# Kernel tuning notes

Measured on AMD Instinct MI355X. Metric: run time of the kernel, lower is better.

## Reference

```python
import jax, jax.numpy as jnp
import numpy as np

B, T, C = 2, 2048, 1024
NH = 16

def setup_inputs() -> dict:
    key = jax.random.key(0)
    ks = jax.random.split(key, 5)
    s = 0.02
    return {
        "x": jax.random.normal(ks[0], (B, T, C), dtype=jnp.float32),
        "w_attn": jax.random.normal(ks[1], (C, 3 * C), dtype=jnp.float32) * s,
        "b_attn": jax.random.normal(ks[2], (3 * C,), dtype=jnp.float32) * s,
        "w_proj": jax.random.normal(ks[3], (C, C), dtype=jnp.float32) * s,
        "b_proj": jax.random.normal(ks[4], (C,), dtype=jnp.float32) * s,
        "n_heads": NH,
    }

def reference(x, w_attn, b_attn, w_proj, b_proj, n_heads):
    Bx, Tx, Cx = x.shape
    hd = Cx // n_heads
    qkv = x @ w_attn + b_attn                      # [B,T,3C]
    q, k, v = jnp.split(qkv, 3, axis=-1)
    # [B,T,H,hd] -> [B,H,T,hd]
    q = q.reshape(Bx, Tx, n_heads, hd).transpose(0, 2, 1, 3)
    k = k.reshape(Bx, Tx, n_heads, hd).transpose(0, 2, 1, 3)
    v = v.reshape(Bx, Tx, n_heads, hd).transpose(0, 2, 1, 3)
    scale = 1.0 / np.sqrt(hd).astype(np.float32)
    att = jnp.einsum('bhqd,bhkd->bhqk', q, k) * scale   # [B,H,T,T]
    causal = jnp.tril(jnp.ones((Tx, Tx), dtype=bool))
    att = jnp.where(causal[None, None], att, -jnp.inf)
    att = jax.nn.softmax(att, axis=-1)
    y = jnp.einsum('bhqk,bhkd->bhqd', att, v)            # [B,H,T,hd]
    y = y.transpose(0, 2, 1, 3).reshape(Bx, Tx, Cx)
    return y @ w_proj + b_proj
```

## Files before the change

kernel.cpp:

```cpp
#include <hip/hip_runtime.h>

typedef __bf16 bf16x8 __attribute__((ext_vector_type(8)));
typedef float  f32x4  __attribute__((ext_vector_type(4)));

#define MFMA_BF16(a, b, c) __builtin_amdgcn_mfma_f32_16x16x32_bf16((a), (b), (c), 0, 0, 0)
#define NEG_INF (-1e30f)
#define SCL 0.18033688f

__device__ __forceinline__ void gld16(const void* g, void* l) {
  __builtin_amdgcn_global_load_lds(
      (const __attribute__((address_space(1))) void*)g,
      (__attribute__((address_space(3))) void*)l, 16, 0, 0);
}

__global__ void cast_f32_bf16(const float* __restrict__ in,
                              __bf16* __restrict__ out, int n) {
  int i = (blockIdx.x * 256 + threadIdx.x) * 8;
  if (i >= n) return;
  float4 a = *(const float4*)&in[i];
  float4 b = *(const float4*)&in[i + 4];
  bf16x8 v;
  v[0] = (__bf16)a.x; v[1] = (__bf16)a.y; v[2] = (__bf16)a.z; v[3] = (__bf16)a.w;
  v[4] = (__bf16)b.x; v[5] = (__bf16)b.y; v[6] = (__bf16)b.z; v[7] = (__bf16)b.w;
  *(bf16x8*)&out[i] = v;
}

__global__ void transpose_f32_bf16(const float* __restrict__ in,
                                   __bf16* __restrict__ out, int R, int C) {
  __shared__ float t[32][33];
  int tx = threadIdx.x & 31, ty = threadIdx.x >> 5;
  int x = blockIdx.x * 32 + tx;
  int y0 = blockIdx.y * 32 + ty;
#pragma unroll
  for (int i = 0; i < 4; ++i)
    t[ty + 8 * i][tx] = in[(size_t)(y0 + 8 * i) * C + x];
  __syncthreads();
  int x2 = blockIdx.y * 32 + tx;
#pragma unroll
  for (int i = 0; i < 4; ++i)
    out[(size_t)(blockIdx.x * 32 + ty + 8 * i) * R + x2] = (__bf16)t[tx][ty + 8 * i];
}

#define BN 128
#define BK 64

template <int BMT, typename TC>
__global__ __launch_bounds__(256) void gemm_bt_bias(
    const __bf16* __restrict__ A, const __bf16* __restrict__ Bt,
    const float* __restrict__ bias, TC* __restrict__ Cmat,
    int M, int N, int K) {
  constexpr int NI = BMT / 32;
  __shared__ __align__(16) __bf16 As[BMT * BK];
  __shared__ __align__(16) __bf16 Bs[BN * BK];
  int tid = threadIdx.x;
  int wave = tid >> 6, lane = tid & 63;
  int l16 = lane & 15, quad = lane >> 4;
  int wm = wave >> 1, wn = wave & 1;
  int m0 = blockIdx.y * BMT, n0 = blockIdx.x * BN;

  f32x4 acc[NI][4];
#pragma unroll
  for (int i = 0; i < NI; ++i)
#pragma unroll
    for (int j = 0; j < 4; ++j) acc[i][j] = (f32x4){0.f, 0.f, 0.f, 0.f};

  int row = tid >> 3;
  int kc = ((tid & 7) ^ ((tid >> 3) & 7)) * 8;
  int xr = (l16 & 7) * 8;

  for (int k0 = 0; k0 < K; k0 += BK) {
#pragma unroll
    for (int i = 0; i < NI; ++i)
      gld16(&A[(size_t)(m0 + row + i * 32) * K + k0 + kc],
            (char*)As + (i * 256 + wave * 64) * 16);
#pragma unroll
    for (int j = 0; j < 4; ++j)
      gld16(&Bt[(size_t)(n0 + row + j * 32) * K + k0 + kc],
            (char*)Bs + (j * 256 + wave * 64) * 16);
    __syncthreads();
#pragma unroll
    for (int ks = 0; ks < 2; ++ks) {
      bf16x8 af[NI], bfr[4];
#pragma unroll
      for (int i = 0; i < NI; ++i)
        af[i] = *(const bf16x8*)&As[(wm * (BMT / 2) + i * 16 + l16) * BK +
                                    ((ks * 32 + quad * 8) ^ xr)];
#pragma unroll
      for (int j = 0; j < 4; ++j)
        bfr[j] = *(const bf16x8*)&Bs[(wn * 64 + j * 16 + l16) * BK +
                                     ((ks * 32 + quad * 8) ^ xr)];
#pragma unroll
      for (int i = 0; i < NI; ++i)
#pragma unroll
        for (int j = 0; j < 4; ++j) acc[i][j] = MFMA_BF16(af[i], bfr[j], acc[i][j]);
    }
    __syncthreads();
  }
#pragma unroll
  for (int i = 0; i < NI; ++i) {
#pragma unroll
    for (int j = 0; j < 4; ++j) {
      int col = n0 + wn * 64 + j * 16 + l16;
      float bv = bias[col];
#pragma unroll
      for (int r = 0; r < 4; ++r) {
        int rw = m0 + wm * (BMT / 2) + i * 16 + quad * 4 + r;
        Cmat[(size_t)rw * N + col] = (TC)(acc[i][j][r] + bv);
      }
    }
  }
}

__global__ __launch_bounds__(256) void attn_causal(
    const __bf16* __restrict__ qkv, __bf16* __restrict__ y) {
  __shared__ __align__(16) __bf16 Kb[2][64 * 72];
  __shared__ __align__(16) __bf16 Vb[2][64 * 72];
  __shared__ __align__(16) __bf16 Ps[4][32 * 72];
  const int tid = threadIdx.x;
  const int wave = tid >> 6, lane = tid & 63;
  const int l16 = lane & 15, quad = lane >> 4;
  const int bh = blockIdx.x;
  const int b = bh >> 4, h = bh & 15;
  const int RS = 3072;
  const int key0 = tid >> 3;
  const int d0 = (tid & 7) * 8;
  const __bf16* kv0 = qkv + (size_t)(b * 2048) * RS + h * 64 + d0;

#pragma unroll 1
  for (int phase = 0; phase < 2; ++phase) {
    const int qt = phase ? (15 - (int)blockIdx.y) : (int)blockIdx.y;
    const int KT = 2 * qt + 2;

    bf16x8 qf[2][2];
#pragma unroll
    for (int t = 0; t < 2; ++t) {
      int qrow = b * 2048 + qt * 128 + wave * 32 + t * 16 + l16;
      const __bf16* qbase = qkv + (size_t)qrow * RS + h * 64;
      qf[t][0] = *(const bf16x8*)(qbase + quad * 8);
      qf[t][1] = *(const bf16x8*)(qbase + 32 + quad * 8);
    }

    float l_i[2][4];
    f32x4 o[2][4];
#pragma unroll
    for (int t = 0; t < 2; ++t)
#pragma unroll
      for (int r = 0; r < 4; ++r) l_i[t][r] = 0.f;
#pragma unroll
    for (int t = 0; t < 2; ++t)
#pragma unroll
      for (int j = 0; j < 4; ++j) o[t][j] = (f32x4){0.f, 0.f, 0.f, 0.f};

    bf16x8 kreg[2], vreg[2];
#pragma unroll
    for (int i = 0; i < 2; ++i) {
      const __bf16* src = kv0 + (size_t)(key0 + 32 * i) * RS;
      kreg[i] = *(const bf16x8*)(src + 1024);
      vreg[i] = *(const bf16x8*)(src + 2048);
    }
#pragma unroll
    for (int i = 0; i < 2; ++i) {
      int key = key0 + 32 * i;
      *(bf16x8*)&Kb[0][key * 72 + d0] = kreg[i];
#pragma unroll
      for (int jj = 0; jj < 8; ++jj)
        Vb[0][(d0 + jj) * 72 + (key ^ d0)] = vreg[i][jj];
    }
    __syncthreads();

    for (int kt = 0; kt < KT; ++kt) {
      const int cur = kt & 1;
      if (kt + 1 < KT) {
#pragma unroll
        for (int i = 0; i < 2; ++i) {
          const __bf16* src = kv0 + (size_t)((kt + 1) * 64 + key0 + 32 * i) * RS;
          kreg[i] = *(const bf16x8*)(src + 1024);
          vreg[i] = *(const bf16x8*)(src + 2048);
        }
      }

      f32x4 s[2][4];
#pragma unroll
      for (int t = 0; t < 2; ++t)
#pragma unroll
        for (int j = 0; j < 4; ++j) s[t][j] = (f32x4){0.f, 0.f, 0.f, 0.f};
#pragma unroll
      for (int j = 0; j < 4; ++j) {
        bf16x8 kf0 = *(const bf16x8*)&Kb[cur][(j * 16 + l16) * 72 + quad * 8];
        bf16x8 kf1 = *(const bf16x8*)&Kb[cur][(j * 16 + l16) * 72 + 32 + quad * 8];
#pragma unroll
        for (int t = 0; t < 2; ++t) {
          s[t][j] = MFMA_BF16(qf[t][0], kf0, s[t][j]);
          s[t][j] = MFMA_BF16(qf[t][1], kf1, s[t][j]);
        }
      }

      if (kt >= 2 * qt) {
        int off = (kt - 2 * qt) * 64;
#pragma unroll
        for (int t = 0; t < 2; ++t) {
          int qg = wave * 32 + t * 16 + quad * 4;
#pragma unroll
          for (int j = 0; j < 4; ++j)
#pragma unroll
            for (int r = 0; r < 4; ++r)
              if (j * 16 + l16 + off > qg + r) s[t][j][r] = NEG_INF;
        }
      }

#pragma unroll
      for (int t = 0; t < 2; ++t)
#pragma unroll
        for (int r = 0; r < 4; ++r)
#pragma unroll
          for (int j = 0; j < 4; ++j) {
            float p = __builtin_amdgcn_exp2f(s[t][j][r] * SCL);
            l_i[t][r] += p;
            Ps[wave][(t * 16 + quad * 4 + r) * 72 + j * 16 + l16] = (__bf16)p;
          }

#pragma unroll
      for (int ks = 0; ks < 2; ++ks) {
        bf16x8 pf[2];
#pragma unroll
        for (int t = 0; t < 2; ++t)
          pf[t] = *(const bf16x8*)&Ps[wave][(t * 16 + l16) * 72 + ks * 32 + quad * 8];
#pragma unroll
        for (int j = 0; j < 4; ++j) {
          int dim = j * 16 + l16;
          bf16x8 vf = *(const bf16x8*)&Vb[cur][dim * 72 + ((ks * 32 + quad * 8) ^ (dim & 56))];
#pragma unroll
          for (int t = 0; t < 2; ++t) o[t][j] = MFMA_BF16(pf[t], vf, o[t][j]);
        }
      }

      if (kt + 1 < KT) {
#pragma unroll
        for (int i = 0; i < 2; ++i) {
          int key = key0 + 32 * i;
          *(bf16x8*)&Kb[cur ^ 1][key * 72 + d0] = kreg[i];
#pragma unroll
          for (int jj = 0; jj < 8; ++jj)
            Vb[cur ^ 1][(d0 + jj) * 72 + (key ^ d0)] = vreg[i][jj];
        }
      }
      __syncthreads();
    }

#pragma unroll
    for (int t = 0; t < 2; ++t) {
      int orow = b * 2048 + qt * 128 + wave * 32 + t * 16 + quad * 4;
#pragma unroll
      for (int r = 0; r < 4; ++r) {
        float l = l_i[t][r];
        l += __shfl_xor(l, 1);
        l += __shfl_xor(l, 2);
        l += __shfl_xor(l, 4);
        l += __shfl_xor(l, 8);
        float inv = 1.f / l;
#pragma unroll
        for (int j = 0; j < 4; ++j)
          y[(size_t)(orow + r) * 1024 + h * 64 + j * 16 + l16] = (__bf16)(o[t][j][r] * inv);
      }
    }
  }
}

extern "C" void kernel_launch(void* const* d_in, const int* in_sizes, int n_in,
                              void* d_out, int out_size, void* d_ws, size_t ws_size,
                              hipStream_t stream) {
  (void)in_sizes; (void)n_in; (void)out_size; (void)ws_size;
  const float* x      = (const float*)d_in[0];
  const float* w_attn = (const float*)d_in[1];
  const float* b_attn = (const float*)d_in[2];
  const float* w_proj = (const float*)d_in[3];
  const float* b_proj = (const float*)d_in[4];
  float* out = (float*)d_out;

  __bf16* wt_attn = (__bf16*)d_ws;
  __bf16* wt_proj = wt_attn + (size_t)3072 * 1024;
  __bf16* qkv     = wt_proj + (size_t)1024 * 1024;
  __bf16* ybuf    = qkv + (size_t)4096 * 3072;

  cast_f32_bf16<<<4096 * 1024 / 2048, 256, 0, stream>>>(x, ybuf, 4096 * 1024);

  transpose_f32_bf16<<<dim3(3072 / 32, 1024 / 32), 256, 0, stream>>>(w_attn, wt_attn, 1024, 3072);
  transpose_f32_bf16<<<dim3(1024 / 32, 1024 / 32), 256, 0, stream>>>(w_proj, wt_proj, 1024, 1024);

  gemm_bt_bias<128, __bf16><<<dim3(3072 / BN, 4096 / 128), 256, 0, stream>>>(
      ybuf, wt_attn, b_attn, qkv, 4096, 3072, 1024);

  attn_causal<<<dim3(2 * 16, 8), 256, 0, stream>>>(qkv, ybuf);

  gemm_bt_bias<64, float><<<dim3(1024 / BN, 4096 / 64), 256, 0, stream>>>(
      ybuf, wt_proj, b_proj, out, 4096, 1024, 1024);
}
```

Measured before the change: 203.7 us.

## Load K tiles via direct global-to-LDS with swizzle and split causal phases into blocks

K tiles are now copied straight from global memory into LDS with global_load_lds into an unpadded, XOR-swizzled layout, removing the register staging and padded stores. The two-phase loop that paired light and heavy query tiles inside one block is replaced by a grid twice as large, with one query tile per block. This raises block-level parallelism but gives up the built-in load balancing, so heavy tiles may form a tail.

Result: faster. 193.9 us (-4.8%).

```diff
diff --git a/kernel.cpp b/kernel.cpp
--- a/kernel.cpp
+++ b/kernel.cpp
@@ -113,7 +113,7 @@
 
 __global__ __launch_bounds__(256) void attn_causal(
     const __bf16* __restrict__ qkv, __bf16* __restrict__ y) {
-  __shared__ __align__(16) __bf16 Kb[2][64 * 72];
+  __shared__ __align__(16) __bf16 Kb[2][64 * 64];
   __shared__ __align__(16) __bf16 Vb[2][64 * 72];
   __shared__ __align__(16) __bf16 Ps[4][32 * 72];
   const int tid = threadIdx.x;
@@ -122,146 +122,145 @@
   const int bh = blockIdx.x;
   const int b = bh >> 4, h = bh & 15;
   const int RS = 3072;
+  const int yb = blockIdx.y;
+  const int qt = (yb < 8) ? yb : 23 - yb;
+  const int KT = 2 * qt + 2;
+
   const int key0 = tid >> 3;
   const int d0 = (tid & 7) * 8;
-  const __bf16* kv0 = qkv + (size_t)(b * 2048) * RS + h * 64 + d0;
-
-#pragma unroll 1
-  for (int phase = 0; phase < 2; ++phase) {
-    const int qt = phase ? (15 - (int)blockIdx.y) : (int)blockIdx.y;
-    const int KT = 2 * qt + 2;
-
-    bf16x8 qf[2][2];
-#pragma unroll
-    for (int t = 0; t < 2; ++t) {
-      int qrow = b * 2048 + qt * 128 + wave * 32 + t * 16 + l16;
-      const __bf16* qbase = qkv + (size_t)qrow * RS + h * 64;
-      qf[t][0] = *(const bf16x8*)(qbase + quad * 8);
-      qf[t][1] = *(const bf16x8*)(qbase + 32 + quad * 8);
-    }
-
-    float l_i[2][4];
-    f32x4 o[2][4];
+  const int kcs = ((tid & 7) ^ ((tid >> 3) & 7)) * 8;
+  const int xr = (l16 & 7) * 8;
+  const __bf16* kbase = qkv + (size_t)(b * 2048) * RS + 1024 + h * 64 + kcs;
+  const __bf16* vbase = qkv + (size_t)(b * 2048) * RS + 2048 + h * 64 + d0;
+
+  bf16x8 qf[2][2];
+#pragma unroll
+  for (int t = 0; t < 2; ++t) {
+    int qrow = b * 2048 + qt * 128 + wave * 32 + t * 16 + l16;
+    const __bf16* qbase = qkv + (size_t)qrow * RS + h * 64;
+    qf[t][0] = *(const bf16x8*)(qbase + quad * 8);
+    qf[t][1] = *(const bf16x8*)(qbase + 32 + quad * 8);
+  }
+
+  float l_i[2][4];
+  f32x4 o[2][4];
+#pragma unroll
+  for (int t = 0; t < 2; ++t)
+#pragma unroll
+    for (int r = 0; r < 4; ++r) l_i[t][r] = 0.f;
+#pragma unroll
+  for (int t = 0; t < 2; ++t)
+#pragma unroll
+    for (int j = 0; j < 4; ++j) o[t][j] = (f32x4){0.f, 0.f, 0.f, 0.f};
+
+  bf16x8 vreg[2];
+#pragma unroll
+  for (int i = 0; i < 2; ++i) {
+    gld16(kbase + (size_t)(key0 + 32 * i) * RS,
+          (char*)Kb[0] + (i * 256 + wave * 64 + lane) * 16);
+    vreg[i] = *(const bf16x8*)(vbase + (size_t)(key0 + 32 * i) * RS);
+  }
+#pragma unroll
+  for (int i = 0; i < 2; ++i) {
+    int key = key0 + 32 * i;
+#pragma unroll
+    for (int jj = 0; jj < 8; ++jj)
+      Vb[0][(d0 + jj) * 72 + (key ^ d0)] = vreg[i][jj];
+  }
+  __syncthreads();
+
+  for (int kt = 0; kt < KT; ++kt) {
+    const int cur = kt & 1;
+    if (kt + 1 < KT) {
+#pragma unroll
+      for (int i = 0; i < 2; ++i) {
+        gld16(kbase + (size_t)((kt + 1) * 64 + key0 + 32 * i) * RS,
+              (char*)Kb[cur ^ 1] + (i * 256 + wave * 64 + lane) * 16);
+        vreg[i] = *(const bf16x8*)(vbase + (size_t)((kt + 1) * 64 + key0 + 32 * i) * RS);
+      }
+    }
+
+    f32x4 s[2][4];
 #pragma unroll
     for (int t = 0; t < 2; ++t)
 #pragma unroll
-      for (int r = 0; r < 4; ++r) l_i[t][r] = 0.f;
+      for (int j = 0; j < 4; ++j) s[t][j] = (f32x4){0.f, 0.f, 0.f, 0.f};
+#pragma unroll
+    for (int j = 0; j < 4; ++j) {
+      bf16x8 kf0 = *(const bf16x8*)&Kb[cur][(j * 16 + l16) * 64 + ((quad * 8) ^ xr)];
+      bf16x8 kf1 = *(const bf16x8*)&Kb[cur][(j * 16 + l16) * 64 + ((32 + quad * 8) ^ xr)];
+#pragma unroll
+      for (int t = 0; t < 2; ++t) {
+        s[t][j] = MFMA_BF16(qf[t][0], kf0, s[t][j]);
+        s[t][j] = MFMA_BF16(qf[t][1], kf1, s[t][j]);
+      }
+    }
+
+    if (kt >= 2 * qt) {
+      int off = (kt - 2 * qt) * 64;
+#pragma unroll
+      for (int t = 0; t < 2; ++t) {
+        int qg = wave * 32 + t * 16 + quad * 4;
+#pragma unroll
+        for (int j = 0; j < 4; ++j)
+#pragma unroll
+          for (int r = 0; r < 4; ++r)
+            if (j * 16 + l16 + off > qg + r) s[t][j][r] = NEG_INF;
+      }
+    }
+
 #pragma unroll
     for (int t = 0; t < 2; ++t)
 #pragma unroll
-      for (int j = 0; j < 4; ++j) o[t][j] = (f32x4){0.f, 0.f, 0.f, 0.f};
-
-    bf16x8 kreg[2], vreg[2];
-#pragma unroll
-    for (int i = 0; i < 2; ++i) {
-      const __bf16* src = kv0 + (size_t)(key0 + 32 * i) * RS;
-      kreg[i] = *(const bf16x8*)(src + 1024);
-      vreg[i] = *(const bf16x8*)(src + 2048);
-    }
-#pragma unroll
-    for (int i = 0; i < 2; ++i) {
-      int key = key0 + 32 * i;
-      *(bf16x8*)&Kb[0][key * 72 + d0] = kreg[i];
-#pragma unroll
-      for (int jj = 0; jj < 8; ++jj)
-        Vb[0][(d0 + jj) * 72 + (key ^ d0)] = vreg[i][jj];
+      for (int r = 0; r < 4; ++r)
+#pragma unroll
+        for (int j = 0; j < 4; ++j) {
+          float p = __builtin_amdgcn_exp2f(s[t][j][r] * SCL);
+          l_i[t][r] += p;
+          Ps[wave][(t * 16 + quad * 4 + r) * 72 + j * 16 + l16] = (__bf16)p;
+        }
+
+#pragma unroll
+    for (int ks = 0; ks < 2; ++ks) {
+      bf16x8 pf[2];
+#pragma unroll
+      for (int t = 0; t < 2; ++t)
+        pf[t] = *(const bf16x8*)&Ps[wave][(t * 16 + l16) * 72 + ks * 32 + quad * 8];
+#pragma unroll
+      for (int j = 0; j < 4; ++j) {
+        int dim = j * 16 + l16;
+        bf16x8 vf = *(const bf16x8*)&Vb[cur][dim * 72 + ((ks * 32 + quad * 8) ^ (dim & 56))];
+#pragma unroll
+        for (int t = 0; t < 2; ++t) o[t][j] = MFMA_BF16(pf[t], vf, o[t][j]);
+      }
+    }
+
+    if (kt + 1 < KT) {
+#pragma unroll
+      for (int i = 0; i < 2; ++i) {
+        int key = key0 + 32 * i;
+#pragma unroll
+        for (int jj = 0; jj < 8; ++jj)
+          Vb[cur ^ 1][(d0 + jj) * 72 + (key ^ d0)] = vreg[i][jj];
+      }
     }
     __syncthreads();
-
-    for (int kt = 0; kt < KT; ++kt) {
-      const int cur = kt & 1;
-      if (kt + 1 < KT) {
-#pragma unroll
-        for (int i = 0; i < 2; ++i) {
-          const __bf16* src = kv0 + (size_t)((kt + 1) * 64 + key0 + 32 * i) * RS;
-          kreg[i] = *(const bf16x8*)(src + 1024);
-          vreg[i] = *(const bf16x8*)(src + 2048);
-        }
-      }
-
-      f32x4 s[2][4];
-#pragma unroll
-      for (int t = 0; t < 2; ++t)
-#pragma unroll
-        for (int j = 0; j < 4; ++j) s[t][j] = (f32x4){0.f, 0.f, 0.f, 0.f};
-#pragma unroll
-      for (int j = 0; j < 4; ++j) {
-        bf16x8 kf0 = *(const bf16x8*)&Kb[cur][(j * 16 + l16) * 72 + quad * 8];
-        bf16x8 kf1 = *(const bf16x8*)&Kb[cur][(j * 16 + l16) * 72 + 32 + quad * 8];
-#pragma unroll
-        for (int t = 0; t < 2; ++t) {
-          s[t][j] = MFMA_BF16(qf[t][0], kf0, s[t][j]);
-          s[t][j] = MFMA_BF16(qf[t][1], kf1, s[t][j]);
-        }
-      }
-
-      if (kt >= 2 * qt) {
-        int off = (kt - 2 * qt) * 64;
-#pragma unroll
-        for (int t = 0; t < 2; ++t) {
-          int qg = wave * 32 + t * 16 + quad * 4;
-#pragma unroll
-          for (int j = 0; j < 4; ++j)
-#pragma unroll
-            for (int r = 0; r < 4; ++r)
-              if (j * 16 + l16 + off > qg + r) s[t][j][r] = NEG_INF;
-        }
-      }
-
-#pragma unroll
-      for (int t = 0; t < 2; ++t)
-#pragma unroll
-        for (int r = 0; r < 4; ++r)
-#pragma unroll
-          for (int j = 0; j < 4; ++j) {
-            float p = __builtin_amdgcn_exp2f(s[t][j][r] * SCL);
-            l_i[t][r] += p;
-            Ps[wave][(t * 16 + quad * 4 + r) * 72 + j * 16 + l16] = (__bf16)p;
-          }
-
-#pragma unroll
-      for (int ks = 0; ks < 2; ++ks) {
-        bf16x8 pf[2];
-#pragma unroll
-        for (int t = 0; t < 2; ++t)
-          pf[t] = *(const bf16x8*)&Ps[wave][(t * 16 + l16) * 72 + ks * 32 + quad * 8];
-#pragma unroll
-        for (int j = 0; j < 4; ++j) {
-          int dim = j * 16 + l16;
-          bf16x8 vf = *(const bf16x8*)&Vb[cur][dim * 72 + ((ks * 32 + quad * 8) ^ (dim & 56))];
-#pragma unroll
-          for (int t = 0; t < 2; ++t) o[t][j] = MFMA_BF16(pf[t], vf, o[t][j]);
-        }
-      }
-
-      if (kt + 1 < KT) {
-#pragma unroll
-        for (int i = 0; i < 2; ++i) {
-          int key = key0 + 32 * i;
-          *(bf16x8*)&Kb[cur ^ 1][key * 72 + d0] = kreg[i];
-#pragma unroll
-          for (int jj = 0; jj < 8; ++jj)
-            Vb[cur ^ 1][(d0 + jj) * 72 + (key ^ d0)] = vreg[i][jj];
-        }
-      }
-      __syncthreads();
-    }
-
-#pragma unroll
-    for (int t = 0; t < 2; ++t) {
-      int orow = b * 2048 + qt * 128 + wave * 32 + t * 16 + quad * 4;
-#pragma unroll
-      for (int r = 0; r < 4; ++r) {
-        float l = l_i[t][r];
-        l += __shfl_xor(l, 1);
-        l += __shfl_xor(l, 2);
-        l += __shfl_xor(l, 4);
-        l += __shfl_xor(l, 8);
-        float inv = 1.f / l;
-#pragma unroll
-        for (int j = 0; j < 4; ++j)
-          y[(size_t)(orow + r) * 1024 + h * 64 + j * 16 + l16] = (__bf16)(o[t][j][r] * inv);
-      }
+  }
+
+#pragma unroll
+  for (int t = 0; t < 2; ++t) {
+    int orow = b * 2048 + qt * 128 + wave * 32 + t * 16 + quad * 4;
+#pragma unroll
+    for (int r = 0; r < 4; ++r) {
+      float l = l_i[t][r];
+      l += __shfl_xor(l, 1);
+      l += __shfl_xor(l, 2);
+      l += __shfl_xor(l, 4);
+      l += __shfl_xor(l, 8);
+      float inv = 1.f / l;
+#pragma unroll
+      for (int j = 0; j < 4; ++j)
+        y[(size_t)(orow + r) * 1024 + h * 64 + j * 16 + l16] = (__bf16)(o[t][j][r] * inv);
     }
   }
 }
@@ -290,7 +289,7 @@
   gemm_bt_bias<128, __bf16><<<dim3(3072 / BN, 4096 / 128), 256, 0, stream>>>(
       ybuf, wt_attn, b_attn, qkv, 4096, 3072, 1024);
 
-  attn_causal<<<dim3(2 * 16, 8), 256, 0, stream>>>(qkv, ybuf);
+  attn_causal<<<dim3(2 * 16, 16), 256, 0, stream>>>(qkv, ybuf);
 
   gemm_bt_bias<64, float><<<dim3(1024 / BN, 4096 / 64), 256, 0, stream>>>(
       ybuf, wt_proj, b_proj, out, 4096, 1024, 1024);
```
